# Optimization experiments

Measured on AMD Instinct MI355X. Metric: run time of the kernel, lower is better.

The kernel has to match this reference:

```python
import jax, jax.numpy as jnp
import numpy as np

# Production-scale dims (see shape_source): time-major, batch must be 1.
T, B, D, S, O, M = 1024, 1, 2048, 1024, 512, 48
TANH_BOUND = 10.0
LN_EPS = 1e-5  # haiku LayerNorm default eps


def setup_inputs() -> dict:
    key = jax.random.key(0)
    ks = jax.random.split(key, 8)

    def lin(k, fin, fout):
        return (jax.random.normal(k, (fin, fout), jnp.float32) / np.float32(np.sqrt(fin)))

    lstm_in = D + 2 * O + S  # concat([inp, error, prev_label]) then concat with h
    return {
        "inputs": jax.random.normal(ks[0], (T, B, D), jnp.float32),
        "labels": jax.random.normal(ks[1], (T, B, O), jnp.float32),
        "W_lstm": lin(ks[2], lstm_in, 4 * S),
        "b_lstm": jnp.zeros((4 * S,), jnp.float32),
        "W_write": lin(ks[3], S, 3 * M + 1),
        "b_write": jnp.zeros((3 * M + 1,), jnp.float32),
        "W_read": lin(ks[4], S, 2 * M),
        "b_read": jnp.zeros((2 * M,), jnp.float32),
        "W_rproj": lin(ks[5], M, S),
        "b_rproj": jnp.zeros((S,), jnp.float32),
        "W_out": lin(ks[6], S, O),
        "b_out": jnp.zeros((O,), jnp.float32),
    }


def _fw_memory(inputs, labels, W_lstm, b_lstm, W_write, b_write,
               W_read, b_read, W_rproj, b_rproj, W_out, b_out):
    Bsz = inputs.shape[1]  # must be 1 (jnp.outer key construction)
    slow = W_lstm.shape[1] // 4
    out_size = W_out.shape[1]
    mem = W_rproj.shape[0]

    h0 = jnp.zeros((Bsz, slow), inputs.dtype)
    c0 = jnp.zeros((Bsz, slow), inputs.dtype)
    mem0 = jnp.zeros((mem, mem * mem), inputs.dtype)
    err0 = jnp.zeros((Bsz, out_size), inputs.dtype)
    lab0 = jnp.zeros((Bsz, out_size), inputs.dtype)

    def tick(carry, x):
        h, c, memory, error, prev_label = carry
        inp, label = x  # [B,D], [B,O]
        # --- LSTM (haiku: forget bias +1) ---
        z = jnp.concatenate([inp, error, prev_label], axis=-1)
        gates = jnp.concatenate([z, h], axis=-1) @ W_lstm + b_lstm  # [B,4S]
        i, g, f, o = jnp.split(gates, 4, axis=-1)
        c = jax.nn.sigmoid(f + 1.0) * c + jax.nn.sigmoid(i) * jnp.tanh(g)
        h = jax.nn.sigmoid(o) * jnp.tanh(c)
        out = h
        # --- rank-1 fast-weight write ---
        write = out @ W_write + b_write                 # [B, 3M+1]
        beta = jax.nn.sigmoid(write[:, -1])             # [B]
        k1, k2, v = jnp.split(jnp.tanh(write[:, :-1]), 3, axis=-1)  # [B,M] each
        key_vec = (k1.reshape(-1)[:, None] * k2.reshape(-1)[None, :]).reshape(-1)  # [M^2]
        v_old = memory @ key_vec                        # [M]
        delta = (v - v_old).reshape(-1)                 # [M]
        memory = memory + beta * (delta[:, None] * key_vec[None, :])
        memory = memory / jnp.maximum(1.0, jnp.linalg.norm(memory))
        # --- rank-1 read + LayerNorm (no scale/offset) ---
        r = jnp.tanh(out @ W_read + b_read)             # [B,2M]
        n, e = jnp.split(r, 2, axis=-1)
        read_key = (n.reshape(-1)[:, None] * e.reshape(-1)[None, :]).reshape(-1)  # [M^2]
        nvec = memory @ read_key                        # [M]
        nvec = (nvec - nvec.mean()) / jnp.sqrt(nvec.var() + LN_EPS)
        readout = nvec @ W_rproj + b_rproj              # [S], broadcast over batch
        out = out + readout
        out = out @ W_out + b_out                       # [B,O]
        out = jnp.tanh(out / TANH_BOUND) * TANH_BOUND
        new_error = out - label  # grad of 0.5*sum((out-label)^2) wrt out
        return (h, c, memory, new_error, label), out

    _, outputs = jax.lax.scan(tick, (h0, c0, mem0, err0, lab0), (inputs, labels))
    return outputs  # [T,B,O]


def reference(inputs, labels, W_lstm, b_lstm, W_write, b_write,
              W_read, b_read, W_rproj, b_rproj, W_out, b_out):
    return _fw_memory(inputs, labels, W_lstm, b_lstm, W_write, b_write,
                      W_read, b_read, W_rproj, b_rproj, W_out, b_out)
```

## Files before the change

kernel.cpp:

```cpp
#include <hip/hip_runtime.h>
#include <math.h>


#define TT 1024
#define DD 2048
#define SS 1024
#define OO 512
#define MM 48
#define NG 4096
#define NWG 256
#define NTHR 256
#define NC 144
#define ND 8

#define W_HP2   0
#define W_ER2   2048
#define W_WR2   3072
#define W_VP2   3584
#define W_NP2   3872
#define W_HW2   4160
#define W_UD2   5184
#define W_IVG2  5280
#define ZERO_WORDS 208256
#define W_PRE    208256
#define W_WWRT  (W_PRE + TT*NG)
#define W_WOUTT (W_WWRT + 241*SS)
#define W_WCOMB (W_WOUTT + OO*SS)
#define W_BCOMB (W_WCOMB + MM*OO)
#define W_WLRP  (W_BCOMB + OO)

typedef unsigned long long u64;

__device__ __forceinline__ u64 ld64(const u64* p) {
  return __hip_atomic_load(p, __ATOMIC_RELAXED, __HIP_MEMORY_SCOPE_AGENT);
}
__device__ __forceinline__ void st64(u64* p, u64 v) {
  __hip_atomic_store(p, v, __ATOMIC_RELAXED, __HIP_MEMORY_SCOPE_AGENT);
}
__device__ __forceinline__ u64 mkpair(float v, int tag) {
  union { float f; unsigned u; } c; c.f = v;
  return (u64)c.u | ((u64)(unsigned)tag << 32);
}
__device__ __forceinline__ float pval(u64 p) {
  union { unsigned u; float f; } c; c.u = (unsigned)p; return c.f;
}
__device__ __forceinline__ int ptag(u64 p) { return (int)(unsigned)(p >> 32); }
__device__ __forceinline__ float spin1(const u64* p, int tag) {
  u64 q = ld64(p);
  while (ptag(q) != tag) { __builtin_amdgcn_s_sleep(1); q = ld64(p); }
  return pval(q);
}
__device__ __forceinline__ float sigm(float x) { return 1.f / (1.f + expf(-x)); }


__global__ void build_wwrT(const float* __restrict__ Ww, const float* __restrict__ Wr,
                           float* __restrict__ wwrT) {
  int id = blockIdx.x * 256 + threadIdx.x;
  if (id < 241 * SS) {
    int d = id >> 10, s = id & 1023;
    wwrT[id] = (d < 145) ? Ww[s * 145 + d] : Wr[s * 96 + (d - 145)];
  }
}

__global__ void build_woutT(const float* __restrict__ Wo, float* __restrict__ woutT) {
  int id = blockIdx.x * 256 + threadIdx.x;
  int o = id >> 10, s = id & 1023;
  woutT[id] = Wo[s * OO + o];
}

__global__ void repack_wl(const float* __restrict__ Wl, float* __restrict__ dst) {
  int id = blockIdx.x * 256 + threadIdx.x;
  int gb = id & 3;
  int r = id >> 2;
  int l = r % 1536;
  int s = r / 1536;
  int wrow = (l < 512) ? (2048 + l) : (2560 + l);
  dst[id] = Wl[(size_t)wrow * NG + gb * 1024 + s];
}

__global__ void wcomb_kernel(const float* __restrict__ Wrp, const float* __restrict__ brp,
                             const float* __restrict__ Wo, const float* __restrict__ bo,
                             float* __restrict__ wcomb, float* __restrict__ bcomb) {
  int id = blockIdx.x * 256 + threadIdx.x;
  int a = id >> 9, o = id & 511;
  if (a < MM) {
    float acc = 0.f;
    for (int s = 0; s < SS; ++s) acc = fmaf(Wrp[a * SS + s], Wo[s * OO + o], acc);
    wcomb[a * OO + o] = acc;
  } else if (a == MM) {
    float acc = bo[o];
    for (int s = 0; s < SS; ++s) acc = fmaf(brp[s], Wo[s * OO + o], acc);
    bcomb[o] = acc;
  }
}

__global__ __launch_bounds__(256)
void pregate_gemm(const float* __restrict__ inp, const float* __restrict__ lab,
                  const float* __restrict__ Wl, const float* __restrict__ bl,
                  float* __restrict__ pre) {
  __shared__ float As[16][65];
  __shared__ float Bs[16][64];
  const int tid = threadIdx.x;
  const int j0 = blockIdx.x * 64;
  const int t0 = blockIdx.y * 64;
  const int tx = tid & 15, ty = tid >> 4;
  float acc[4][4] = {};
  for (int kc = 0; kc < 2560; kc += 16) {
    __syncthreads();
#pragma unroll
    for (int p = 0; p < 4; ++p) {
      int id = tid + p * 256;
      int r = id >> 4, kk = id & 15;
      int t = t0 + r, k = kc + kk;
      float v;
      if (k < DD) v = inp[(size_t)t * DD + k];
      else v = (t > 0) ? lab[(size_t)(t - 1) * OO + (k - DD)] : 0.f;
      As[kk][r] = v;
      int kr = id >> 6, j = id & 63;
      int k2 = kc + kr;
      int wrow = (k2 < DD) ? k2 : (512 + k2);
      Bs[kr][j] = Wl[(size_t)wrow * NG + j0 + j];
    }
    __syncthreads();
#pragma unroll
    for (int kk = 0; kk < 16; ++kk) {
      float av[4], bv[4];
#pragma unroll
      for (int i = 0; i < 4; ++i) av[i] = As[kk][ty * 4 + i];
#pragma unroll
      for (int i = 0; i < 4; ++i) bv[i] = Bs[kk][tx * 4 + i];
#pragma unroll
      for (int i = 0; i < 4; ++i)
#pragma unroll
        for (int jx = 0; jx < 4; ++jx) acc[i][jx] = fmaf(av[i], bv[jx], acc[i][jx]);
    }
  }
#pragma unroll
  for (int i = 0; i < 4; ++i) {
    int t = t0 + ty * 4 + i;
#pragma unroll
    for (int jx = 0; jx < 4; ++jx) {
      int j = j0 + tx * 4 + jx;
      pre[(size_t)t * NG + j] = acc[i][jx] + bl[j];
    }
  }
}


__global__ __launch_bounds__(NTHR, 1)
void persistent_kernel(float* ws, const float* __restrict__ labels,
                       const float* __restrict__ bwv, const float* __restrict__ brv,
                       float* __restrict__ out) {
  u64* const hp2 = (u64*)(ws + W_HP2);
  u64* const er2 = (u64*)(ws + W_ER2);
  u64* const wr2 = (u64*)(ws + W_WR2);
  u64* const vp2 = (u64*)(ws + W_VP2);
  u64* const np2 = (u64*)(ws + W_NP2);
  u64* const hw2 = (u64*)(ws + W_HW2);
  u64* const ud2 = (u64*)(ws + W_UD2);
  u64* const iv2 = (u64*)(ws + W_IVG2);
  const float* const pre = ws + W_PRE;
  const float* const wwrT = ws + W_WWRT;
  const float* const woutT = ws + W_WOUTT;
  const float* const wcomb = ws + W_WCOMB;
  const float* const bcomb = ws + W_BCOMB;

  const int w = blockIdx.x;
  const int tid = threadIdx.x;
  const int sc = tid >> 6;
  const int rl = tid & 63;
  const float4* const blk4 =
      (const float4*)(ws + W_WLRP) + (size_t)w * 6144 + (size_t)sc * 1536;

  const bool isC = (w < NC);
  const bool isD = (w >= NC && w < NC + ND);
  const int ca = w / 3, cch = w % 3;
  const int dbase = (w - NC) * 64;
  const int p_ = w - (NC + ND);

  float4 werr[8], whh[16];
#pragma unroll
  for (int it = 0; it < 8; ++it) werr[it] = blk4[rl + it * 64];
#pragma unroll
  for (int it = 0; it < 16; ++it) whh[it] = blk4[512 + rl + it * 64];

  int slot = -1;
  float wreg[16];
  float breg = 0.f;
  if (p_ >= 0) {
    int s_ = p_ * 4 + sc;
    if (s_ < 241) slot = s_;
  }
  if (slot >= 0) {
    const float* wrow = wwrT + (size_t)slot * SS;
#pragma unroll
    for (int i = 0; i < 16; ++i) wreg[i] = wrow[rl + 64 * i];
    breg = (slot < 145) ? bwv[slot] : brv[slot - 145];
  }
  const int hslot = (p_ >= 0) ? (p_ * 4 + sc) : -1;

  float creg = 0.f;
  float ah0 = 0.f, ah1 = 0.f, ah2 = 0.f, ah3 = 0.f;
  float labr = 0.f;
  float m2c = 0.f;

  __shared__ float pg2[2][16];
  __shared__ float errs[512];
  __shared__ float hlds[1024];
  __shared__ float t1[96], t2[96], s3[49];
  __shared__ float nvln_s[MM];
  __shared__ float wcl[MM * 64];
  __shared__ float Mlds[768];
  __shared__ float vps[144], nps[144], hws[64];
  __shared__ float cred[2][4];
  __shared__ float shud[2];

  if (isD) {
    for (int i = tid; i < MM * 64; i += NTHR)
      wcl[i] = wcomb[(size_t)(i >> 6) * OO + dbase + (i & 63)];
    if (tid < 64) labr = labels[dbase + tid];
  }
  float hbias = 0.f;
  if (isD && tid < 64) hbias = bcomb[dbase + tid];
  if (tid < 16)
    pg2[0][tid] = pre[(size_t)(tid >> 2) * 1024 + w * 4 + (tid & 3)];
#pragma unroll
  for (int i = 0; i < 3; ++i) Mlds[tid + i * 256] = 0.f;
  errs[tid] = 0.f; errs[tid + 256] = 0.f;
  __syncthreads();

  for (int t = 0; t < TT; ++t) {
    __syncthreads();

    if (t > 0) {
      if (tid < 64) {
        u64 pr[8];
        for (;;) {
#pragma unroll
          for (int i = 0; i < 8; ++i) pr[i] = ld64(er2 + tid + i * 64);
          int bad = 0;
#pragma unroll
          for (int i = 0; i < 8; ++i) bad |= (ptag(pr[i]) != t);
          if (!bad) break;
          __builtin_amdgcn_s_sleep(1);
        }
#pragma unroll
        for (int i = 0; i < 8; ++i) errs[tid + i * 64] = pval(pr[i]);
      }
      __syncthreads();
    }
    {
      float a0 = ah0, a1 = ah1, a2 = ah2, a3 = ah3;
#pragma unroll
      for (int it = 0; it < 8; ++it) {
        float xv = errs[rl + it * 64];
        a0 = fmaf(xv, werr[it].x, a0);
        a1 = fmaf(xv, werr[it].y, a1);
        a2 = fmaf(xv, werr[it].z, a2);
        a3 = fmaf(xv, werr[it].w, a3);
      }
#pragma unroll
      for (int off = 32; off; off >>= 1) {
        a0 += __shfl_down(a0, off, 64);
        a1 += __shfl_down(a1, off, 64);
        a2 += __shfl_down(a2, off, 64);
        a3 += __shfl_down(a3, off, 64);
      }
      if (rl == 0) {
        const float* pgc = pg2[t & 1];
        float gi = a0 + pgc[0 + sc];
        float gg = a1 + pgc[4 + sc];
        float gf = a2 + pgc[8 + sc];
        float go = a3 + pgc[12 + sc];
        creg = sigm(gf + 1.f) * creg + sigm(gi) * tanhf(gg);
        float hn = sigm(go) * tanhf(creg);
        st64(hp2 + w * 4 + sc, mkpair(hn, t + 1));
      }
    }

    if (isC) {
      if (t > 0) {
        if (tid == 0) { shud[0] = spin1(ud2 + ca, t); shud[1] = spin1(iv2, t); }
        __syncthreads();
        float uda = shud[0], ivgr = shud[1];
#pragma unroll
        for (int i = 0; i < 3; ++i) {
          int c = tid + i * 256;
          int gc = cch * 768 + c;
          int a2 = gc / 48, b2 = gc - a2 * 48;
          Mlds[c] = Mlds[c] * ivgr + uda * (t1[a2] * t1[48 + b2]);
        }
      }
      if (tid < 64) {
        u64 ph[16];
        for (;;) {
#pragma unroll
          for (int i = 0; i < 16; ++i) ph[i] = ld64(hp2 + tid + i * 64);
          int bad = 0;
#pragma unroll
          for (int i = 0; i < 16; ++i) bad |= (ptag(ph[i]) != t + 1);
          if (!bad) break;
          __builtin_amdgcn_s_sleep(1);
        }
#pragma unroll
        for (int i = 0; i < 16; ++i) hlds[tid + i * 64] = pval(ph[i]);
      }
      __syncthreads();
      if (tid < 192) {
        int di = (tid < 96) ? tid : (tid + 49);
        u64 pr = ld64(wr2 + di);
        while (ptag(pr) != t + 1) {
          __builtin_amdgcn_s_sleep(2);
          pr = ld64(wr2 + di);
        }
        if (tid < 96) t1[tid] = pval(pr); else t2[tid - 96] = pval(pr);
      }
      __syncthreads();
      {
        float sk = 0.f, sr = 0.f;
#pragma unroll
        for (int i = 0; i < 3; ++i) {
          int c = tid + i * 256;
          int gc = cch * 768 + c;
          int a2 = gc / 48, b2 = gc - a2 * 48;
          float m = Mlds[c];
          sk = fmaf(m, t1[a2] * t1[48 + b2], sk);
          sr = fmaf(m, t2[a2] * t2[48 + b2], sr);
        }
#pragma unroll
        for (int off = 32; off; off >>= 1) {
          sk += __shfl_down(sk, off, 64);
          sr += __shfl_down(sr, off, 64);
        }
        if (rl == 0) { cred[0][sc] = sk; cred[1][sc] = sr; }
        __syncthreads();
        if (tid == 0) {
          st64(vp2 + ca * 3 + cch,
               mkpair(cred[0][0] + cred[0][1] + cred[0][2] + cred[0][3], t + 1));
          st64(np2 + ca * 3 + cch,
               mkpair(cred[1][0] + cred[1][1] + cred[1][2] + cred[1][3], t + 1));
        }
      }
    } else if (isD) {
      if (tid < 64) {
        u64 ph[16];
        for (;;) {
#pragma unroll
          for (int i = 0; i < 16; ++i) ph[i] = ld64(hp2 + tid + i * 64);
          int bad = 0;
#pragma unroll
          for (int i = 0; i < 16; ++i) bad |= (ptag(ph[i]) != t + 1);
          if (!bad) break;
          __builtin_amdgcn_s_sleep(1);
        }
#pragma unroll
        for (int i = 0; i < 16; ++i) hlds[tid + i * 64] = pval(ph[i]);
      }
      __syncthreads();
      {
        float b0 = 0.f, b1 = 0.f, b2 = 0.f, b3 = 0.f;
#pragma unroll
        for (int it = 0; it < 16; ++it) {
          float xv = hlds[rl + it * 64];
          b0 = fmaf(xv, whh[it].x, b0);
          b1 = fmaf(xv, whh[it].y, b1);
          b2 = fmaf(xv, whh[it].z, b2);
          b3 = fmaf(xv, whh[it].w, b3);
        }
        ah0 = b0; ah1 = b1; ah2 = b2; ah3 = b3;
      }
      if (tid < 16 && t + 1 < TT)
        pg2[(t + 1) & 1][tid] =
            pre[(size_t)(t + 1) * NG + (tid >> 2) * 1024 + w * 4 + (tid & 3)];
      float labr2 = 0.f;
      if (tid < 64 && t + 1 < TT)
        labr2 = labels[(size_t)(t + 1) * OO + dbase + tid];
      {
        const int i0 = tid, i1 = tid + 256, i2 = tid + 512;
        const bool h1 = (i1 < 593), h2 = (i2 < 593);
        auto paddr = [&](int idx) -> u64* {
          if (idx < 241) return wr2 + idx;
          if (idx < 385) return vp2 + (idx - 241);
          if (idx < 529) return np2 + (idx - 385);
          return hw2 + dbase + (idx - 529);
        };
        u64 q0, q1 = 0, q2 = 0;
        for (;;) {
          q0 = ld64(paddr(i0));
          if (h1) q1 = ld64(paddr(i1));
          if (h2) q2 = ld64(paddr(i2));
          int bad = (ptag(q0) != t + 1);
          if (h1) bad |= (ptag(q1) != t + 1);
          if (h2) bad |= (ptag(q2) != t + 1);
          if (!bad) break;
          __builtin_amdgcn_s_sleep(1);
        }
        auto route = [&](int idx, float v) {
          if (idx < 96) t1[idx] = v;
          else if (idx < 144) s3[idx - 96] = v;
          else if (idx == 144) s3[48] = v;
          else if (idx < 241) t2[idx - 145] = v;
          else if (idx < 385) vps[idx - 241] = v;
          else if (idx < 529) nps[idx - 385] = v;
          else hws[idx - 529] = v;
        };
        route(i0, pval(q0));
        if (h1) route(i1, pval(q1));
        if (h2) route(i2, pval(q2));
      }
      __syncthreads();
      if (tid < 64) {
        const int a = tid;
        const bool va = a < MM;
        float lv = 0.f, d = 0.f, t1a = 0.f, t1b = 0.f, t2a = 0.f, t2b = 0.f;
        float ln = 0.f;
        if (va) {
          lv = vps[3 * a] + vps[3 * a + 1] + vps[3 * a + 2];
          ln = nps[3 * a] + nps[3 * a + 1] + nps[3 * a + 2];
          d = s3[a] - lv;
          t1a = t1[a]; t1b = t1[48 + a];
          t2a = t2[a]; t2b = t2[48 + a];
        }
        float beta = sigm(s3[48]);
        float sdv = va ? d * lv : 0.f;
        float sdd = va ? d * d : 0.f;
        float sk1 = va ? t1a * t1a : 0.f;
        float sk2 = va ? t1b * t1b : 0.f;
        float skn = va ? t1a * t2a : 0.f;
        float ske = va ? t1b * t2b : 0.f;
#pragma unroll
        for (int off = 32; off; off >>= 1) {
          sdv += __shfl_down(sdv, off, 64);
          sdd += __shfl_down(sdd, off, 64);
          sk1 += __shfl_down(sk1, off, 64);
          sk2 += __shfl_down(sk2, off, 64);
          skn += __shfl_down(skn, off, 64);
          ske += __shfl_down(ske, off, 64);
        }
        sdv = __shfl(sdv, 0, 64);
        sdd = __shfl(sdd, 0, 64);
        sk1 = __shfl(sk1, 0, 64);
        sk2 = __shfl(sk2, 0, 64);
        skn = __shfl(skn, 0, 64);
        ske = __shfl(ske, 0, 64);
        float n2 = m2c + 2.f * beta * sdv + beta * beta * sdd * (sk1 * sk2);
        float n2c = fmaxf(n2, 0.f);
        m2c = fminf(n2c, 1.f);
        float gam = sqrtf(n2c);
        if (gam < 1.f) gam = 1.f;
        float ivg = 1.f / gam;
        float kdr = skn * ske;
        float nv = va ? (ln + beta * d * kdr) * ivg : 0.f;
        float mean = nv, msq = nv * nv;
#pragma unroll
        for (int off = 32; off; off >>= 1) {
          mean += __shfl_down(mean, off, 64);
          msq += __shfl_down(msq, off, 64);
        }
        mean = __shfl(mean, 0, 64) * (1.f / 48.f);
        msq = __shfl(msq, 0, 64) * (1.f / 48.f);
        float rstd = rsqrtf(msq - mean * mean + 1e-5f);
        if (va) nvln_s[a] = (nv - mean) * rstd;
        if (w == NC) {
          if (va) st64(ud2 + a, mkpair(beta * ivg * d, t + 1));
          if (tid == 0) st64(iv2, mkpair(ivg, t + 1));
        }
      }
      __syncthreads();
      if (tid < 64) {
        float acc = hws[tid] + hbias;
#pragma unroll 8
        for (int a = 0; a < MM; ++a) acc = fmaf(nvln_s[a], wcl[a * 64 + tid], acc);
        float y = 10.f * tanhf(acc * 0.1f);
        out[(size_t)t * OO + dbase + tid] = y;
        st64(er2 + dbase + tid, mkpair(y - labr, t + 1));
      }
      labr = labr2;
    } else {
      if (tid < 64) {
        u64 ph[16];
        for (;;) {
#pragma unroll
          for (int i = 0; i < 16; ++i) ph[i] = ld64(hp2 + tid + i * 64);
          int bad = 0;
#pragma unroll
          for (int i = 0; i < 16; ++i) bad |= (ptag(ph[i]) != t + 1);
          if (!bad) break;
          __builtin_amdgcn_s_sleep(1);
        }
#pragma unroll
        for (int i = 0; i < 16; ++i) hlds[tid + i * 64] = pval(ph[i]);
      }
      __syncthreads();
      float hv[16];
#pragma unroll
      for (int i = 0; i < 16; ++i) hv[i] = hlds[rl + i * 64];
      if (slot >= 0) {
        float acc = 0.f;
#pragma unroll
        for (int i = 0; i < 16; ++i) acc = fmaf(hv[i], wreg[i], acc);
#pragma unroll
        for (int off = 32; off; off >>= 1) acc += __shfl_down(acc, off, 64);
        if (rl == 0) {
          float dv = acc + breg;
          st64(wr2 + slot, mkpair((slot == 144) ? dv : tanhf(dv), t + 1));
        }
      }
      {
        const float* wrow = woutT + (size_t)hslot * SS;
        float acc = 0.f;
#pragma unroll
        for (int i = 0; i < 16; ++i)
          acc = fmaf(hv[i], wrow[rl + i * 64], acc);
#pragma unroll
        for (int off = 32; off; off >>= 1) acc += __shfl_down(acc, off, 64);
        if (rl == 0) st64(hw2 + hslot, mkpair(acc, t + 1));
        if (hslot < 96) {
          int o2 = hslot + 416;
          const float* wrow2 = woutT + (size_t)o2 * SS;
          float ac2 = 0.f;
#pragma unroll
          for (int i = 0; i < 16; ++i)
            ac2 = fmaf(hv[i], wrow2[rl + i * 64], ac2);
#pragma unroll
          for (int off = 32; off; off >>= 1) ac2 += __shfl_down(ac2, off, 64);
          if (rl == 0) st64(hw2 + o2, mkpair(ac2, t + 1));
        }
      }
    }

    if (!isD) {
      float b0 = 0.f, b1 = 0.f, b2 = 0.f, b3 = 0.f;
#pragma unroll
      for (int it = 0; it < 16; ++it) {
        float xv = hlds[rl + it * 64];
        b0 = fmaf(xv, whh[it].x, b0);
        b1 = fmaf(xv, whh[it].y, b1);
        b2 = fmaf(xv, whh[it].z, b2);
        b3 = fmaf(xv, whh[it].w, b3);
      }
      ah0 = b0; ah1 = b1; ah2 = b2; ah3 = b3;
      if (tid < 16 && t + 1 < TT)
        pg2[(t + 1) & 1][tid] =
            pre[(size_t)(t + 1) * NG + (tid >> 2) * 1024 + w * 4 + (tid & 3)];
    }
  }
}

extern "C" void kernel_launch(void* const* d_in, const int* in_sizes, int n_in,
                              void* d_out, int out_size, void* d_ws, size_t ws_size,
                              hipStream_t stream) {
  const float* inp = (const float*)d_in[0];
  const float* lab = (const float*)d_in[1];
  const float* Wl = (const float*)d_in[2];
  const float* bl = (const float*)d_in[3];
  const float* Ww = (const float*)d_in[4];
  const float* bw = (const float*)d_in[5];
  const float* Wr = (const float*)d_in[6];
  const float* br = (const float*)d_in[7];
  const float* Wrp = (const float*)d_in[8];
  const float* brp = (const float*)d_in[9];
  const float* Wo = (const float*)d_in[10];
  const float* bo = (const float*)d_in[11];
  float* ws = (float*)d_ws;
  float* outp = (float*)d_out;
  (void)in_sizes; (void)n_in; (void)out_size; (void)ws_size;

  hipMemsetAsync(d_ws, 0, (size_t)ZERO_WORDS * 4, stream);
  hipLaunchKernelGGL(build_wwrT, dim3((241 * SS + 255) / 256), dim3(256), 0, stream,
                     Ww, Wr, ws + W_WWRT);
  hipLaunchKernelGGL(build_woutT, dim3(OO * SS / 256), dim3(256), 0, stream,
                     Wo, ws + W_WOUTT);
  hipLaunchKernelGGL(repack_wl, dim3(1536 * NG / 256), dim3(256), 0, stream,
                     Wl, ws + W_WLRP);
  hipLaunchKernelGGL(wcomb_kernel, dim3(98), dim3(256), 0, stream,
                     Wrp, brp, Wo, bo, ws + W_WCOMB, ws + W_BCOMB);
  hipLaunchKernelGGL(pregate_gemm, dim3(64, 16), dim3(256), 0, stream,
                     inp, lab, Wl, bl, ws + W_PRE);
  hipLaunchKernelGGL(persistent_kernel, dim3(NWG), dim3(NTHR), 0, stream,
                     ws, lab, bw, br, outp);
}
```

Before: 14.65 ms.

## Replicate output/error computation in every workgroup to remove error broadcast round trip

Removes the dedicated D workgroups that computed the LayerNorm, the output projection and the error vector and then broadcast them through global memory. Every workgroup now spins on the write/read/partial-sum slots itself, recomputes the memory-norm/LayerNorm scalars and the full 512-wide error vector locally, and keeps the combined projection weights in registers. The h vector is held in registers per lane rather than staged through shared memory, and the W_out rows are preloaded into registers. This cuts one cross-workgroup dependency hop per timestep, at the cost of redundant per-block work, heavier register pressure, and all 256 blocks polling the same global slots.

New measurement: 14.92 ms. No clear change (+1.8%).

```diff
diff --git a/kernel.cpp b/kernel.cpp
--- a/kernel.cpp
+++ b/kernel.cpp
@@ -11,16 +11,13 @@
 #define NWG 256
 #define NTHR 256
 #define NC 144
-#define ND 8
+#define NSPIN 529
 
 #define W_HP2   0
-#define W_ER2   2048
 #define W_WR2   3072
 #define W_VP2   3584
 #define W_NP2   3872
 #define W_HW2   4160
-#define W_UD2   5184
-#define W_IVG2  5280
 #define ZERO_WORDS 208256
 #define W_PRE    208256
 #define W_WWRT  (W_PRE + TT*NG)
@@ -152,13 +149,10 @@
                        const float* __restrict__ bwv, const float* __restrict__ brv,
                        float* __restrict__ out) {
   u64* const hp2 = (u64*)(ws + W_HP2);
-  u64* const er2 = (u64*)(ws + W_ER2);
   u64* const wr2 = (u64*)(ws + W_WR2);
   u64* const vp2 = (u64*)(ws + W_VP2);
   u64* const np2 = (u64*)(ws + W_NP2);
   u64* const hw2 = (u64*)(ws + W_HW2);
-  u64* const ud2 = (u64*)(ws + W_UD2);
-  u64* const iv2 = (u64*)(ws + W_IVG2);
   const float* const pre = ws + W_PRE;
   const float* const wwrT = ws + W_WWRT;
   const float* const woutT = ws + W_WOUTT;
@@ -173,82 +167,88 @@
       (const float4*)(ws + W_WLRP) + (size_t)w * 6144 + (size_t)sc * 1536;
 
   const bool isC = (w < NC);
-  const bool isD = (w >= NC && w < NC + ND);
   const int ca = w / 3, cch = w % 3;
-  const int dbase = (w - NC) * 64;
-  const int p_ = w - (NC + ND);
+  const int g = (w - NC) * 4 + sc;
 
   float4 werr[8], whh[16];
 #pragma unroll
   for (int it = 0; it < 8; ++it) werr[it] = blk4[rl + it * 64];
 #pragma unroll
-  for (int it = 0; it < 16; ++it) whh[it] = blk4[512 + rl + it * 64];
+  for (int it = 0; it < 16; ++it) whh[it] = blk4[512 + it * 64 + rl];
+
+  float wc0[48], wc1[48];
+#pragma unroll
+  for (int a = 0; a < 48; ++a) {
+    wc0[a] = wcomb[(size_t)a * OO + tid];
+    wc1[a] = wcomb[(size_t)a * OO + tid + 256];
+  }
+  const float bc0 = bcomb[tid], bc1 = bcomb[tid + 256];
 
   int slot = -1;
   float wreg[16];
   float breg = 0.f;
-  if (p_ >= 0) {
-    int s_ = p_ * 4 + sc;
-    if (s_ < 241) slot = s_;
-  }
-  if (slot >= 0) {
+  if (!isC && g < 241) {
+    slot = g;
     const float* wrow = wwrT + (size_t)slot * SS;
 #pragma unroll
     for (int i = 0; i < 16; ++i) wreg[i] = wrow[rl + 64 * i];
     breg = (slot < 145) ? bwv[slot] : brv[slot - 145];
   }
-  const int hslot = (p_ >= 0) ? (p_ * 4 + sc) : -1;
+  float wh1[16], wh2[16];
+  int o2 = -1;
+  if (!isC) {
+    const float* wrow = woutT + (size_t)g * SS;
+#pragma unroll
+    for (int i = 0; i < 16; ++i) wh1[i] = wrow[rl + 64 * i];
+    if (g < 64) {
+      o2 = g + 448;
+      const float* wrow2 = woutT + (size_t)o2 * SS;
+#pragma unroll
+      for (int i = 0; i < 16; ++i) wh2[i] = wrow2[rl + 64 * i];
+    }
+  }
 
   float creg = 0.f;
   float ah0 = 0.f, ah1 = 0.f, ah2 = 0.f, ah3 = 0.f;
-  float labr = 0.f;
   float m2c = 0.f;
+  float zb0 = 0.f, zb1 = 0.f;
+  float lab0 = 0.f, lab1 = 0.f;
 
   __shared__ float pg2[2][16];
   __shared__ float errs[512];
-  __shared__ float hlds[1024];
   __shared__ float t1[96], t2[96], s3[49];
-  __shared__ float nvln_s[MM];
-  __shared__ float wcl[MM * 64];
+  __shared__ float nvln_s[48];
+  __shared__ float vps[144], nps[144];
   __shared__ float Mlds[768];
-  __shared__ float vps[144], nps[144], hws[64];
   __shared__ float cred[2][4];
   __shared__ float shud[2];
 
-  if (isD) {
-    for (int i = tid; i < MM * 64; i += NTHR)
-      wcl[i] = wcomb[(size_t)(i >> 6) * OO + dbase + (i & 63)];
-    if (tid < 64) labr = labels[dbase + tid];
-  }
-  float hbias = 0.f;
-  if (isD && tid < 64) hbias = bcomb[dbase + tid];
   if (tid < 16)
     pg2[0][tid] = pre[(size_t)(tid >> 2) * 1024 + w * 4 + (tid & 3)];
+  errs[tid] = 0.f; errs[tid + 256] = 0.f;
 #pragma unroll
   for (int i = 0; i < 3; ++i) Mlds[tid + i * 256] = 0.f;
-  errs[tid] = 0.f; errs[tid + 256] = 0.f;
   __syncthreads();
 
   for (int t = 0; t < TT; ++t) {
     __syncthreads();
 
     if (t > 0) {
-      if (tid < 64) {
-        u64 pr[8];
-        for (;;) {
-#pragma unroll
-          for (int i = 0; i < 8; ++i) pr[i] = ld64(er2 + tid + i * 64);
-          int bad = 0;
-#pragma unroll
-          for (int i = 0; i < 8; ++i) bad |= (ptag(pr[i]) != t);
-          if (!bad) break;
-          __builtin_amdgcn_s_sleep(1);
-        }
-#pragma unroll
-        for (int i = 0; i < 8; ++i) errs[tid + i * 64] = pval(pr[i]);
-      }
+      float acc0 = zb0, acc1 = zb1;
+#pragma unroll
+      for (int a = 0; a < 48; ++a) {
+        acc0 = fmaf(nvln_s[a], wc0[a], acc0);
+        acc1 = fmaf(nvln_s[a], wc1[a], acc1);
+      }
+      float y0 = 10.f * tanhf(acc0 * 0.1f);
+      float y1 = 10.f * tanhf(acc1 * 0.1f);
+      errs[tid] = y0 - lab0;
+      errs[tid + 256] = y1 - lab1;
+      if (w == NC) out[(size_t)(t - 1) * OO + tid] = y0;
+      else if (w == NC + 1) out[(size_t)(t - 1) * OO + tid + 256] = y1;
       __syncthreads();
     }
+
     {
       float a0 = ah0, a1 = ah1, a2 = ah2, a3 = ah3;
 #pragma unroll
@@ -278,10 +278,9 @@
       }
     }
 
+    float hv[16];
     if (isC) {
       if (t > 0) {
-        if (tid == 0) { shud[0] = spin1(ud2 + ca, t); shud[1] = spin1(iv2, t); }
-        __syncthreads();
         float uda = shud[0], ivgr = shud[1];
 #pragma unroll
         for (int i = 0; i < 3; ++i) {
@@ -291,11 +290,11 @@
           Mlds[c] = Mlds[c] * ivgr + uda * (t1[a2] * t1[48 + b2]);
         }
       }
-      if (tid < 64) {
+      {
         u64 ph[16];
         for (;;) {
 #pragma unroll
-          for (int i = 0; i < 16; ++i) ph[i] = ld64(hp2 + tid + i * 64);
+          for (int i = 0; i < 16; ++i) ph[i] = ld64(hp2 + rl + i * 64);
           int bad = 0;
 #pragma unroll
           for (int i = 0; i < 16; ++i) bad |= (ptag(ph[i]) != t + 1);
@@ -303,7 +302,7 @@
           __builtin_amdgcn_s_sleep(1);
         }
 #pragma unroll
-        for (int i = 0; i < 16; ++i) hlds[tid + i * 64] = pval(ph[i]);
+        for (int i = 0; i < 16; ++i) hv[i] = pval(ph[i]);
       }
       __syncthreads();
       if (tid < 192) {
@@ -341,12 +340,12 @@
                mkpair(cred[1][0] + cred[1][1] + cred[1][2] + cred[1][3], t + 1));
         }
       }
-    } else if (isD) {
-      if (tid < 64) {
+    } else {
+      {
         u64 ph[16];
         for (;;) {
 #pragma unroll
-          for (int i = 0; i < 16; ++i) ph[i] = ld64(hp2 + tid + i * 64);
+          for (int i = 0; i < 16; ++i) ph[i] = ld64(hp2 + rl + i * 64);
           int bad = 0;
 #pragma unroll
           for (int i = 0; i < 16; ++i) bad |= (ptag(ph[i]) != t + 1);
@@ -354,147 +353,8 @@
           __builtin_amdgcn_s_sleep(1);
         }
 #pragma unroll
-        for (int i = 0; i < 16; ++i) hlds[tid + i * 64] = pval(ph[i]);
-      }
-      __syncthreads();
-      {
-        float b0 = 0.f, b1 = 0.f, b2 = 0.f, b3 = 0.f;
-#pragma unroll
-        for (int it = 0; it < 16; ++it) {
-          float xv = hlds[rl + it * 64];
-          b0 = fmaf(xv, whh[it].x, b0);
-          b1 = fmaf(xv, whh[it].y, b1);
-          b2 = fmaf(xv, whh[it].z, b2);
-          b3 = fmaf(xv, whh[it].w, b3);
-        }
-        ah0 = b0; ah1 = b1; ah2 = b2; ah3 = b3;
-      }
-      if (tid < 16 && t + 1 < TT)
-        pg2[(t + 1) & 1][tid] =
-            pre[(size_t)(t + 1) * NG + (tid >> 2) * 1024 + w * 4 + (tid & 3)];
-      float labr2 = 0.f;
-      if (tid < 64 && t + 1 < TT)
-        labr2 = labels[(size_t)(t + 1) * OO + dbase + tid];
-      {
-        const int i0 = tid, i1 = tid + 256, i2 = tid + 512;
-        const bool h1 = (i1 < 593), h2 = (i2 < 593);
-        auto paddr = [&](int idx) -> u64* {
-          if (idx < 241) return wr2 + idx;
-          if (idx < 385) return vp2 + (idx - 241);
-          if (idx < 529) return np2 + (idx - 385);
-          return hw2 + dbase + (idx - 529);
-        };
-        u64 q0, q1 = 0, q2 = 0;
-        for (;;) {
-          q0 = ld64(paddr(i0));
-          if (h1) q1 = ld64(paddr(i1));
-          if (h2) q2 = ld64(paddr(i2));
-          int bad = (ptag(q0) != t + 1);
-          if (h1) bad |= (ptag(q1) != t + 1);
-          if (h2) bad |= (ptag(q2) != t + 1);
-          if (!bad) break;
-          __builtin_amdgcn_s_sleep(1);
-        }
-        auto route = [&](int idx, float v) {
-          if (idx < 96) t1[idx] = v;
-          else if (idx < 144) s3[idx - 96] = v;
-          else if (idx == 144) s3[48] = v;
-          else if (idx < 241) t2[idx - 145] = v;
-          else if (idx < 385) vps[idx - 241] = v;
-          else if (idx < 529) nps[idx - 385] = v;
-          else hws[idx - 529] = v;
-        };
-        route(i0, pval(q0));
-        if (h1) route(i1, pval(q1));
-        if (h2) route(i2, pval(q2));
-      }
-      __syncthreads();
-      if (tid < 64) {
-        const int a = tid;
-        const bool va = a < MM;
-        float lv = 0.f, d = 0.f, t1a = 0.f, t1b = 0.f, t2a = 0.f, t2b = 0.f;
-        float ln = 0.f;
-        if (va) {
-          lv = vps[3 * a] + vps[3 * a + 1] + vps[3 * a + 2];
-          ln = nps[3 * a] + nps[3 * a + 1] + nps[3 * a + 2];
-          d = s3[a] - lv;
-          t1a = t1[a]; t1b = t1[48 + a];
-          t2a = t2[a]; t2b = t2[48 + a];
-        }
-        float beta = sigm(s3[48]);
-        float sdv = va ? d * lv : 0.f;
-        float sdd = va ? d * d : 0.f;
-        float sk1 = va ? t1a * t1a : 0.f;
-        float sk2 = va ? t1b * t1b : 0.f;
-        float skn = va ? t1a * t2a : 0.f;
-        float ske = va ? t1b * t2b : 0.f;
-#pragma unroll
-        for (int off = 32; off; off >>= 1) {
-          sdv += __shfl_down(sdv, off, 64);
-          sdd += __shfl_down(sdd, off, 64);
-          sk1 += __shfl_down(sk1, off, 64);
-          sk2 += __shfl_down(sk2, off, 64);
-          skn += __shfl_down(skn, off, 64);
-          ske += __shfl_down(ske, off, 64);
-        }
-        sdv = __shfl(sdv, 0, 64);
-        sdd = __shfl(sdd, 0, 64);
-        sk1 = __shfl(sk1, 0, 64);
-        sk2 = __shfl(sk2, 0, 64);
-        skn = __shfl(skn, 0, 64);
-        ske = __shfl(ske, 0, 64);
-        float n2 = m2c + 2.f * beta * sdv + beta * beta * sdd * (sk1 * sk2);
-        float n2c = fmaxf(n2, 0.f);
-        m2c = fminf(n2c, 1.f);
-        float gam = sqrtf(n2c);
-        if (gam < 1.f) gam = 1.f;
-        float ivg = 1.f / gam;
-        float kdr = skn * ske;
-        float nv = va ? (ln + beta * d * kdr) * ivg : 0.f;
-        float mean = nv, msq = nv * nv;
-#pragma unroll
-        for (int off = 32; off; off >>= 1) {
-          mean += __shfl_down(mean, off, 64);
-          msq += __shfl_down(msq, off, 64);
-        }
-        mean = __shfl(mean, 0, 64) * (1.f / 48.f);
-        msq = __shfl(msq, 0, 64) * (1.f / 48.f);
-        float rstd = rsqrtf(msq - mean * mean + 1e-5f);
-        if (va) nvln_s[a] = (nv - mean) * rstd;
-        if (w == NC) {
-          if (va) st64(ud2 + a, mkpair(beta * ivg * d, t + 1));
-          if (tid == 0) st64(iv2, mkpair(ivg, t + 1));
-        }
-      }
-      __syncthreads();
-      if (tid < 64) {
-        float acc = hws[tid] + hbias;
-#pragma unroll 8
-        for (int a = 0; a < MM; ++a) acc = fmaf(nvln_s[a], wcl[a * 64 + tid], acc);
-        float y = 10.f * tanhf(acc * 0.1f);
-        out[(size_t)t * OO + dbase + tid] = y;
-        st64(er2 + dbase + tid, mkpair(y - labr, t + 1));
-      }
-      labr = labr2;
-    } else {
-      if (tid < 64) {
-        u64 ph[16];
-        for (;;) {
-#pragma unroll
-          for (int i = 0; i < 16; ++i) ph[i] = ld64(hp2 + tid + i * 64);
-          int bad = 0;
-#pragma unroll
-          for (int i = 0; i < 16; ++i) bad |= (ptag(ph[i]) != t + 1);
-          if (!bad) break;
-          __builtin_amdgcn_s_sleep(1);
-        }
-#pragma unroll
-        for (int i = 0; i < 16; ++i) hlds[tid + i * 64] = pval(ph[i]);
-      }
-      __syncthreads();
-      float hv[16];
-#pragma unroll
-      for (int i = 0; i < 16; ++i) hv[i] = hlds[rl + i * 64];
+        for (int i = 0; i < 16; ++i) hv[i] = pval(ph[i]);
+      }
       if (slot >= 0) {
         float acc = 0.f;
 #pragma unroll
@@ -507,21 +367,16 @@
         }
       }
       {
-        const float* wrow = woutT + (size_t)hslot * SS;
         float acc = 0.f;
 #pragma unroll
-        for (int i = 0; i < 16; ++i)
-          acc = fmaf(hv[i], wrow[rl + i * 64], acc);
+        for (int i = 0; i < 16; ++i) acc = fmaf(hv[i], wh1[i], acc);
 #pragma unroll
         for (int off = 32; off; off >>= 1) acc += __shfl_down(acc, off, 64);
-        if (rl == 0) st64(hw2 + hslot, mkpair(acc, t + 1));
-        if (hslot < 96) {
-          int o2 = hslot + 416;
-          const float* wrow2 = woutT + (size_t)o2 * SS;
+        if (rl == 0) st64(hw2 + g, mkpair(acc, t + 1));
+        if (o2 >= 0) {
           float ac2 = 0.f;
 #pragma unroll
-          for (int i = 0; i < 16; ++i)
-            ac2 = fmaf(hv[i], wrow2[rl + i * 64], ac2);
+          for (int i = 0; i < 16; ++i) ac2 = fmaf(hv[i], wh2[i], ac2);
 #pragma unroll
           for (int off = 32; off; off >>= 1) ac2 += __shfl_down(ac2, off, 64);
           if (rl == 0) st64(hw2 + o2, mkpair(ac2, t + 1));
@@ -529,21 +384,127 @@
       }
     }
 
-    if (!isD) {
+    {
       float b0 = 0.f, b1 = 0.f, b2 = 0.f, b3 = 0.f;
 #pragma unroll
       for (int it = 0; it < 16; ++it) {
-        float xv = hlds[rl + it * 64];
+        float xv = hv[it];
         b0 = fmaf(xv, whh[it].x, b0);
         b1 = fmaf(xv, whh[it].y, b1);
         b2 = fmaf(xv, whh[it].z, b2);
         b3 = fmaf(xv, whh[it].w, b3);
       }
       ah0 = b0; ah1 = b1; ah2 = b2; ah3 = b3;
-      if (tid < 16 && t + 1 < TT)
-        pg2[(t + 1) & 1][tid] =
-            pre[(size_t)(t + 1) * NG + (tid >> 2) * 1024 + w * 4 + (tid & 3)];
-    }
+    }
+    if (tid < 16 && t + 1 < TT)
+      pg2[(t + 1) & 1][tid] =
+          pre[(size_t)(t + 1) * NG + (tid >> 2) * 1024 + w * 4 + (tid & 3)];
+    lab0 = labels[(size_t)t * OO + tid];
+    lab1 = labels[(size_t)t * OO + tid + 256];
+    zb0 = bc0 + spin1(hw2 + tid, t + 1);
+    zb1 = bc1 + spin1(hw2 + tid + 256, t + 1);
+
+    {
+      const int i0 = tid, i1 = tid + 256, i2 = tid + 512;
+      const bool h2 = (i2 < NSPIN);
+      auto paddr = [&](int idx) -> const u64* {
+        if (idx < 241) return wr2 + idx;
+        if (idx < 385) return vp2 + (idx - 241);
+        return np2 + (idx - 385);
+      };
+      u64 q0, q1, q2 = 0;
+      for (;;) {
+        q0 = ld64(paddr(i0));
+        q1 = ld64(paddr(i1));
+        if (h2) q2 = ld64(paddr(i2));
+        int bad = (ptag(q0) != t + 1) | (ptag(q1) != t + 1);
+        if (h2) bad |= (ptag(q2) != t + 1);
+        if (!bad) break;
+        __builtin_amdgcn_s_sleep(1);
+      }
+      auto route = [&](int idx, float v) {
+        if (idx < 96) t1[idx] = v;
+        else if (idx < 144) s3[idx - 96] = v;
+        else if (idx == 144) s3[48] = v;
+        else if (idx < 241) t2[idx - 145] = v;
+        else if (idx < 385) vps[idx - 241] = v;
+        else nps[idx - 385] = v;
+      };
+      route(i0, pval(q0));
+      route(i1, pval(q1));
+      if (h2) route(i2, pval(q2));
+    }
+    __syncthreads();
+    if (tid < 64) {
+      const int a = tid;
+      const bool va = a < MM;
+      float lv = 0.f, d = 0.f, t1a = 0.f, t1b = 0.f, t2a = 0.f, t2b = 0.f;
+      float ln = 0.f;
+      if (va) {
+        lv = vps[3 * a] + vps[3 * a + 1] + vps[3 * a + 2];
+        ln = nps[3 * a] + nps[3 * a + 1] + nps[3 * a + 2];
+        d = s3[a] - lv;
+        t1a = t1[a]; t1b = t1[48 + a];
+        t2a = t2[a]; t2b = t2[48 + a];
+      }
+      float beta = sigm(s3[48]);
+      float sdv = va ? d * lv : 0.f;
+      float sdd = va ? d * d : 0.f;
+      float sk1 = va ? t1a * t1a : 0.f;
+      float sk2 = va ? t1b * t1b : 0.f;
+      float skn = va ? t1a * t2a : 0.f;
+      float ske = va ? t1b * t2b : 0.f;
+#pragma unroll
+      for (int off = 32; off; off >>= 1) {
+        sdv += __shfl_down(sdv, off, 64);
+        sdd += __shfl_down(sdd, off, 64);
+        sk1 += __shfl_down(sk1, off, 64);
+        sk2 += __shfl_down(sk2, off, 64);
+        skn += __shfl_down(skn, off, 64);
+        ske += __shfl_down(ske, off, 64);
+      }
+      sdv = __shfl(sdv, 0, 64);
+      sdd = __shfl(sdd, 0, 64);
+      sk1 = __shfl(sk1, 0, 64);
+      sk2 = __shfl(sk2, 0, 64);
+      skn = __shfl(skn, 0, 64);
+      ske = __shfl(ske, 0, 64);
+      float n2 = m2c + 2.f * beta * sdv + beta * beta * sdd * (sk1 * sk2);
+      float n2c = fmaxf(n2, 0.f);
+      m2c = fminf(n2c, 1.f);
+      float gam = sqrtf(n2c);
+      if (gam < 1.f) gam = 1.f;
+      float ivg = 1.f / gam;
+      float kdr = skn * ske;
+      float nv = va ? (ln + beta * d * kdr) * ivg : 0.f;
+      float mean = nv, msq = nv * nv;
+#pragma unroll
+      for (int off = 32; off; off >>= 1) {
+        mean += __shfl_down(mean, off, 64);
+        msq += __shfl_down(msq, off, 64);
+      }
+      mean = __shfl(mean, 0, 64) * (1.f / 48.f);
+      msq = __shfl(msq, 0, 64) * (1.f / 48.f);
+      float rstd = rsqrtf(msq - mean * mean + 1e-5f);
+      if (va) nvln_s[a] = (nv - mean) * rstd;
+      if (isC) {
+        if (a == ca) shud[0] = beta * ivg * d;
+        if (tid == 0) shud[1] = ivg;
+      }
+    }
+  }
+
+  __syncthreads();
+  {
+    float acc0 = zb0, acc1 = zb1;
+#pragma unroll
+    for (int a = 0; a < 48; ++a) {
+      acc0 = fmaf(nvln_s[a], wc0[a], acc0);
+      acc1 = fmaf(nvln_s[a], wc1[a], acc1);
+    }
+    if (w == NC) out[(size_t)(TT - 1) * OO + tid] = 10.f * tanhf(acc0 * 0.1f);
+    else if (w == NC + 1)
+      out[(size_t)(TT - 1) * OO + tid + 256] = 10.f * tanhf(acc1 * 0.1f);
   }
 }
 
```
